# Optimization experiments

Hardware: AMD Instinct MI355X
Metric: run time of the kernel (lower is better)

The kernel has to match this reference:

```python
import jax, jax.numpy as jnp
import numpy as np
from jax import lax

NEG = -jnp.inf


def _lse(x):
    # safe logsumexp over last axis: rows of all -inf give -inf with zero grads
    m = lax.stop_gradient(jnp.max(x, axis=-1, keepdims=True))
    m = jnp.where(jnp.isfinite(m), m, 0.0)
    s = jnp.sum(jnp.exp(x - m), axis=-1)
    return jnp.where(s > 0, jnp.log(jnp.where(s > 0, s, 1.0)), NEG) + m[..., 0]


def _inside(s_arc, s_sib, mask):
    # s_arc[b, dep, head]; s_sib[b, dep, head, sib]; mask[b, s] (col 0 False)
    B, S, _ = s_arc.shape
    A = jnp.transpose(s_arc, (0, 2, 1))        # [b, head, dep]
    SB = jnp.transpose(s_sib, (0, 2, 1, 3))    # [b, head, dep, sib]
    lens = jnp.sum(mask.astype(jnp.int32), axis=1)
    k = jnp.arange(S)[:, None]   # span start index (stripe row)
    j = jnp.arange(S)[None, :]   # offset within stripe (split/sibling)
    d = jnp.arange(S)
    s_i0 = jnp.full((B, S, S), NEG, dtype=s_arc.dtype)  # incomplete spans [b, head, dep]
    s_s0 = s_i0                                          # sibling spans
    s_c0 = s_i0.at[:, d, d].set(0.0)                     # complete spans, width-0 = 0

    def step(carry, w):
        s_i, s_s, s_c = carry
        valid = (k < S - w) & (j < w)
        kw, kj, kj1 = k + w, k + j, k + j + 1
        # left incomplete: I(k+w -> k), siblings at k+1+j
        il = s_i[:, kw, kj1] + s_s[:, kj1, k] + SB[:, kw, k, kj1]
        il = jnp.where(valid, il, NEG)
        il0 = jnp.where(k == 0, 0.0, s_c[:, kw, kw] + s_c[:, k, kw - 1])  # [B,S,1]
        il = jnp.where(j == w - 1, il0, il)
        s_i = jnp.where(k - j == w, _lse(il)[:, None, :] + A, s_i)
        # right incomplete: I(k -> k+w), siblings at k+j (row k=0 forbidden)
        ir = s_i[:, k, kj] + s_s[:, kj, kw] + SB[:, k, kw, kj]
        ir = jnp.where(valid & (k > 0), ir, NEG)
        ir0 = s_c[:, k, k] + s_c[:, kw, k + 1]
        ir = jnp.where(j == 0, ir0, ir)
        s_i = jnp.where(j - k == w, _lse(ir)[:, :, None] + A, s_i)
        # sibling spans S(k, k+w)
        slr = jnp.where(valid, s_c[:, k, kj] + s_c[:, kw, kj1], NEG)
        sl = _lse(slr)
        s_s = jnp.where(k - j == w, sl[:, None, :], s_s)
        s_s = jnp.where(j - k == w, sl[:, :, None], s_s)
        # complete spans (use s_i updated at this width)
        cl = jnp.where(valid, s_c[:, kj, k] + s_i[:, kw, kj], NEG)
        cr = jnp.where(valid, s_i[:, k, kj1] + s_c[:, kj1, kw], NEG)
        s_c = jnp.where(k - j == w, _lse(cl)[:, None, :], s_c)
        s_c = jnp.where(j - k == w, _lse(cr)[:, :, None], s_c)
        # single-root constraint: kill C(0 -> w) for sentences of length != w
        row0 = jnp.where((d[None, :] == w) & (lens[:, None] != w), NEG, s_c[:, 0, :])
        s_c = s_c.at[:, 0, :].set(row0)
        return (s_i, s_s, s_c), None

    (_, _, s_c), _ = lax.scan(jax.checkpoint(step), (s_i0, s_s0, s_c0), jnp.arange(1, S))
    logZ = jnp.take_along_axis(s_c[:, 0, :], lens[:, None], axis=1).sum()
    return logZ


def setup_inputs() -> dict:
    B, S = 16, 128
    key = jax.random.key(0)
    k1, k2, k3, k4 = jax.random.split(key, 4)
    s_arc = jax.random.normal(k1, (B, S, S), jnp.float32)
    s_sib = jax.random.normal(k2, (B, S, S, S), jnp.float32)
    mask = jnp.ones((B, S), bool).at[:, 0].set(False)
    arcs = jax.random.randint(k3, (B, S), 0, S, jnp.int32)
    sibs = jax.random.randint(k4, (B, S, S), 0, S, jnp.int32)
    return {"s_arc": s_arc, "s_sib": s_sib, "mask": mask, "arcs": arcs, "sibs": sibs}


def reference(s_arc, s_sib, mask, arcs, sibs):
    logZ = _inside(s_arc, s_sib, mask)
    arc_sel = jnp.take_along_axis(s_arc, arcs[:, :, None], axis=-1)[..., 0]
    score = jnp.where(mask, arc_sel, 0.0).sum()
    sib_sel = jnp.take_along_axis(s_sib, sibs[..., None], axis=-1)[..., 0]
    score = score + jnp.where(sibs > 0, sib_sel, 0.0).sum()
    loss = (logZ - score) / mask.sum()
    return loss
```

## Files before the change

### kernel.cpp

```cpp
#include <hip/hip_runtime.h>

#define S 128
#define NEGF (-1e30f)
#define MAXB 16
#define NT 1024
#define STAGE_SZ 8064
#define PKB 700000

__device__ float g_ssw[MAXB * S * S];
__device__ float g_spk[(size_t)MAXB * PKB];
__device__ float g_logZ[MAXB];
__device__ float g_partials[512];

__device__ __forceinline__ bool mask_at(const unsigned char* m, int i, bool by) {
  return by ? (m[i] != 0) : (((const int*)m)[i] != 0);
}

__device__ __forceinline__ void gload_lds4(const float* g, float* l) {
  __builtin_amdgcn_global_load_lds(
      (const __attribute__((address_space(1))) unsigned int*)g,
      (__attribute__((address_space(3))) unsigned int*)l, 4, 0, 0);
}

__device__ __forceinline__ void upd(float& m, float& s, float v) {
  float mn = fmaxf(m, v);
  s = s * __expf(m - mn) + __expf(v - mn);
  m = mn;
}
__device__ __forceinline__ void fold(float& m0, float& s0, float m1, float s1) {
  float mn = fmaxf(m0, m1);
  s0 = s0 * __expf(m0 - mn) + s1 * __expf(m1 - mn);
  m0 = mn;
}
template <int CTRL>
__device__ __forceinline__ float dpp_f(float x) {
  int i = __float_as_int(x);
  return __int_as_float(__builtin_amdgcn_update_dpp(i, i, CTRL, 0xF, 0xF, false));
}
__device__ __forceinline__ void xfold(float& m, float& s, int lp) {
  if (lp >= 1) { float mo = dpp_f<0xB1>(m),  so = dpp_f<0xB1>(s);  fold(m, s, mo, so); }
  if (lp >= 2) { float mo = dpp_f<0x4E>(m),  so = dpp_f<0x4E>(s);  fold(m, s, mo, so); }
  if (lp >= 3) { float mo = dpp_f<0x141>(m), so = dpp_f<0x141>(s); fold(m, s, mo, so); }
  if (lp >= 4) { float mo = dpp_f<0x140>(m), so = dpp_f<0x140>(s); fold(m, s, mo, so); }
}
template <typename F>
__device__ __forceinline__ void lse_acc(F val, int i0, int n, float& M, float& Ss) {
  int i = i0;
  const int ie = i0 + n;
  for (; i + 8 <= ie; i += 8) {
    float v0 = val(i),     v1 = val(i + 1), v2 = val(i + 2), v3 = val(i + 3),
          v4 = val(i + 4), v5 = val(i + 5), v6 = val(i + 6), v7 = val(i + 7);
    float mc = fmaxf(fmaxf(fmaxf(v0, v1), fmaxf(v2, v3)),
                     fmaxf(fmaxf(v4, v5), fmaxf(v6, v7)));
    float s8 = ((__expf(v0 - mc) + __expf(v1 - mc)) +
                (__expf(v2 - mc) + __expf(v3 - mc))) +
               ((__expf(v4 - mc) + __expf(v5 - mc)) +
                (__expf(v6 - mc) + __expf(v7 - mc)));
    float mn = fmaxf(M, mc);
    Ss = Ss * __expf(M - mn) + s8 * __expf(mc - mn);
    M = mn;
  }
  for (; i < ie; ++i) upd(M, Ss, val(i));
}
template <typename F>
__device__ __forceinline__ float lse_c8(F val, int i0, int n, int lp) {
  float M = NEGF, Ss = 0.f;
  lse_acc(val, i0, n, M, Ss);
  xfold(M, Ss, lp);
  return __logf(Ss) + M;
}
__device__ __forceinline__ int lp_cap(int cap) {
  return cap >= 16 ? 4 : cap >= 8 ? 3 : cap >= 4 ? 2 : cap >= 2 ? 1 : 0;
}

__global__ __launch_bounds__(256) void pack_kernel(const float* __restrict__ sib) {
  const int wn = 2 + (blockIdx.x % 126);
  const int b = blockIdx.x / 126;
  const int nk2 = S - wn;
  const int rows1 = nk2 - 1;
  if (rows1 <= 0) return;
  const int rowlen = wn - 1;
  const int rlP = rowlen | 1;
  int off = 0;
  for (int v = 2; v < wn; ++v) off += 2 * (S - v - 1) * ((v - 1) | 1);
  const float* SBraw = sib + (size_t)b * S * S * S;
  float* dst = g_spk + (size_t)b * PKB + off;
  const int lane5 = threadIdx.x & 31;
  const int R = 2 * rows1;
  for (int r = (threadIdx.x >> 5); r < R; r += 8) {
    const int typ = (r >= rows1) ? 1 : 0;
    const int kr = (r - typ * rows1) + 1;
    const int kw2 = kr + wn;
    const size_t srcoff = (typ == 0)
        ? ((size_t)(kw2 * S + kr) * S + (kr + 1))
        : ((size_t)(kr * S + kw2) * S + (kr + 1));
    const float* src = SBraw + srcoff;
    float* d = dst + r * rlP;
    for (int i = lane5; i < rowlen; i += 32) d[i] = src[i];
  }
}

__global__ __launch_bounds__(NT) void dp_kernel(
    const float* __restrict__ arc,
    const unsigned char* __restrict__ mask)
{
  __shared__ float si[S][S];
  __shared__ float sc[S][S];
  __shared__ float stage[STAGE_SZ];
  __shared__ int len_sh, cnt0_sh;

  const int b = blockIdx.x;
  const int tid = threadIdx.x;
  const float* arc_b = arc + (size_t)b * S * S;
  const float* spk_b = g_spk + (size_t)b * PKB;
  float* ssw = g_ssw + (size_t)b * S * S;

  if (tid == 0) { len_sh = 0; cnt0_sh = 0; }
  __syncthreads();
  if (tid < S && mask[tid] != 0) atomicAdd(&cnt0_sh, 1);
  for (int i = tid; i < S * S; i += NT) {
    (&si[0][0])[i] = NEGF;
    (&sc[0][0])[i] = NEGF;
  }
  __syncthreads();
  const bool bytes = (cnt0_sh >= 64);
  if (tid < S) {
    sc[tid][tid] = 0.0f;
    if (mask_at(mask, b * S + tid, bytes)) atomicAdd(&len_sh, 1);
  }
  __syncthreads();
  const int len = min(len_sh, S - 1);
  if (tid == 0) g_logZ[b] = 0.0f;

  float mP = NEGF, sP = 0.f, arcvP = 0.f;
  if (tid >= 512) {
    const int fam = (tid >= 768);
    const int floc = tid & 255;
    const int lp = lp_cap(256 / (S - 1));
    const int k = floc >> lp;
    if (k < S - 1)
      arcvP = fam ? arc_b[k * S + (k + 1)] : arc_b[(k + 1) * S + k];
  }

  int spk_off = 0;

  for (int w = 1; w < S; ++w) {
    const int nk = S - w;
    const int wn = w + 1;

    if (wn < S) {
      const int rows1n = S - wn - 1;
      const int T = 2 * rows1n * ((wn - 1) | 1);
      const float* src = spk_b + spk_off;
      const int wv = tid >> 6, l = tid & 63;
      for (int c = wv; c * 64 < T; c += 16) {
        const int e = c * 64 + l;
        if (e < T) gload_lds4(src + e, &stage[c * 64]);
      }
      spk_off += T;
    }

    if (tid < 512) {
      const int lp = lp_cap(512 / nk);
      const int p = 1 << lp;
      const int q = tid & (p - 1);
      const int k = tid >> lp;
      if (k >= 1 && k < nk) {
        const int kw = k + w;
        const float* ra = &sc[k][k];
        const float* rb = &sc[kw][k + 1];
        const int ch = w >> lp;
        const int i0 = q * ch;
        const int n = ((q == p - 1) ? w : i0 + ch) - i0;
        auto val = [&](int i) { return ra[i] + rb[i]; };
        float r = lse_c8(val, i0, n, lp);
        if (q == 0) ssw[w * S + k] = r;
      }
    } else {
      const int fam = (tid >= 768);
      const int floc = tid & 255;
      const int lp = lp_cap(256 / nk);
      const int p = 1 << lp;
      const int q = floc & (p - 1);
      const int k = floc >> lp;
      if (k < nk) {
        const int kw = k + w;
        float bm;
        if (fam == 0) bm = sc[k][k] + sc[kw][k + 1];
        else bm = (k == 0) ? 0.0f : (sc[kw][kw] + sc[k][kw - 1]);
        float m = mP, s = sP;
        if (q == 0) fold(m, s, bm, 1.0f);
        xfold(m, s, lp);
        if (q == 0) {
          const float r = __logf(s) + m + arcvP;
          if (fam == 0) si[k][kw] = r;
          else          si[kw][k] = r;
        }
      }
    }
    __syncthreads();

    if (tid < 512) {
      const int fam = (tid >= 256);
      const int floc = tid & 255;
      const int lp = lp_cap(256 / nk);
      const int p = 1 << lp;
      const int q = floc & (p - 1);
      const int k = floc >> lp;
      if (k < nk) {
        const int kw = k + w;
        const int ch = w >> lp;
        const int i0 = q * ch;
        const int n = ((q == p - 1) ? w : i0 + ch) - i0;
        if (fam == 0) {
          const float* pA = &sc[k][k];
          const float* pB = &si[kw][k];
          auto val = [&](int i) { return pA[i * S] + pB[i]; };
          float r = lse_c8(val, i0, n, lp);
          if (q == 0) sc[kw][k] = r;
        } else {
          const float* pA = &si[k][k + 1];
          const float* pB = &sc[k + 1][kw];
          auto val = [&](int i) { return pA[i] + pB[i * S]; };
          float r = lse_c8(val, i0, n, lp);
          if (q == 0) {
            if (k == 0) {
              if (w == len) g_logZ[b] = r;
              sc[0][w] = (w == len) ? r : NEGF;
            } else {
              sc[k][kw] = r;
            }
          }
        }
      }
    } else {
      mP = NEGF; sP = 0.f; arcvP = 0.f;
      if (wn < S) {
        const int fam = (tid >= 768);
        const int floc = tid & 255;
        const int nk2 = S - wn;
        const int lp = lp_cap(256 / nk2);
        const int p = 1 << lp;
        const int q = floc & (p - 1);
        const int k = floc >> lp;
        if (k < nk2) {
          const int kw2 = k + wn;
          arcvP = (fam == 0) ? arc_b[kw2 * S + k] : arc_b[k * S + kw2];
          if (k >= 1) {
            const int n1n = wn - 1;
            const int rlPn = n1n | 1;
            const float *pa, *pt, *pw;
            int wstr;
            if (fam == 0) {
              pa = &si[k][k + 1];
              pt = &stage[(k - 1) * rlPn];
              pw = ssw + n1n * S + (k + 1);
              wstr = 1 - S;
            } else {
              pa = &si[kw2][k + 1];
              pt = &stage[((nk2 - 1) + (k - 1)) * rlPn];
              pw = ssw + S + k;
              wstr = S;
            }
            const int ch = n1n >> lp;
            const int i0 = q * ch;
            const int n = ((q == p - 1) ? n1n : i0 + ch) - i0;
            auto val = [&](int i) { return pa[i] + pt[i] + pw[i * wstr]; };
            lse_acc(val, i0, n, mP, sP);
          }
        }
      }
    }
    __syncthreads();
  }
}

__global__ __launch_bounds__(256) void score_kernel(
    const float* __restrict__ arc, const float* __restrict__ sib,
    const unsigned char* __restrict__ mask, const int* __restrict__ arcs,
    const int* __restrict__ sibs, int B)
{
  __shared__ bool bytes_sh;
  if (threadIdx.x == 0) {
    int c = 0;
    for (int i = 0; i < S; ++i) c += (mask[i] != 0);
    bytes_sh = (c >= 64);
  }
  __syncthreads();
  const bool bytes = bytes_sh;

  const int total = B * S * S;
  int tid = blockIdx.x * blockDim.x + threadIdx.x;
  float sum = 0.f, cnt = 0.f;
  for (int e = tid; e < total; e += gridDim.x * blockDim.x) {
    int sv = sibs[e];
    if (sv > 0) sum += sib[(size_t)e * S + sv];
    if ((e & (S - 1)) == 0) {
      int bi = e >> 7;
      if (mask_at(mask, bi, bytes)) { sum += arc[(size_t)bi * S + arcs[bi]]; cnt += 1.f; }
    }
  }
  __shared__ float rs[256], rc[256];
  rs[threadIdx.x] = sum; rc[threadIdx.x] = cnt;
  __syncthreads();
  for (int off = 128; off; off >>= 1) {
    if (threadIdx.x < off) {
      rs[threadIdx.x] += rs[threadIdx.x + off];
      rc[threadIdx.x] += rc[threadIdx.x + off];
    }
    __syncthreads();
  }
  if (threadIdx.x == 0) {
    g_partials[blockIdx.x * 2]     = rs[0];
    g_partials[blockIdx.x * 2 + 1] = rc[0];
  }
}

__global__ __launch_bounds__(256) void final_kernel(int B, float* __restrict__ out)
{
  __shared__ float rs[256], rc[256];
  int t = threadIdx.x;
  float v = -g_partials[t * 2];
  float c = g_partials[t * 2 + 1];
  if (t < B) v += g_logZ[t];
  rs[t] = v; rc[t] = c;
  __syncthreads();
  for (int off = 128; off; off >>= 1) {
    if (t < off) { rs[t] += rs[t + off]; rc[t] += rc[t + off]; }
    __syncthreads();
  }
  if (t == 0) out[0] = rs[0] / rc[0];
}

extern "C" void kernel_launch(void* const* d_in, const int* in_sizes, int n_in,
                              void* d_out, int out_size, void* d_ws, size_t ws_size,
                              hipStream_t stream) {
  const float* s_arc = (const float*)d_in[0];
  const float* s_sib = (const float*)d_in[1];
  const unsigned char* mask = (const unsigned char*)d_in[2];
  const int* arcs = (const int*)d_in[3];
  const int* sibs = (const int*)d_in[4];
  int B = in_sizes[0] / (S * S);
  if (B > MAXB) B = MAXB;

  pack_kernel<<<dim3(B * 126), dim3(256), 0, stream>>>(s_sib);
  score_kernel<<<dim3(256), dim3(256), 0, stream>>>(s_arc, s_sib, mask, arcs, sibs, B);
  dp_kernel<<<dim3(B), dim3(NT), 0, stream>>>(s_arc, mask);
  final_kernel<<<dim3(1), dim3(256), 0, stream>>>(B, (float*)d_out);
}
```

Before: 547.3 us.

## Transpose packed sibling scores and read them directly from global memory

The pack kernel now writes sibling scores transposed, with an LDS tile transpose, so that consecutive k values are contiguous for each split index i. The DP kernel drops the per-width global-to-LDS staging buffer and its async loads and reads the packed data straight from global memory, so lanes over k coalesce. The accumulation helpers are also respecialised with compile-time strides instead of lambdas. This removes LDS staging traffic and shared-memory footprint but puts global-memory latency directly on the inner lse loop and grows the packed buffer.

```diff
diff --git a/kernel.cpp b/kernel.cpp
--- a/kernel.cpp
+++ b/kernel.cpp
@@ -4,22 +4,15 @@
 #define NEGF (-1e30f)
 #define MAXB 16
 #define NT 1024
-#define STAGE_SZ 8064
-#define PKB 700000
+#define PKB2 2080000
 
 __device__ float g_ssw[MAXB * S * S];
-__device__ float g_spk[(size_t)MAXB * PKB];
+__device__ float g_spk2[(size_t)MAXB * PKB2];
 __device__ float g_logZ[MAXB];
 __device__ float g_partials[512];
 
 __device__ __forceinline__ bool mask_at(const unsigned char* m, int i, bool by) {
   return by ? (m[i] != 0) : (((const int*)m)[i] != 0);
-}
-
-__device__ __forceinline__ void gload_lds4(const float* g, float* l) {
-  __builtin_amdgcn_global_load_lds(
-      (const __attribute__((address_space(1))) unsigned int*)g,
-      (__attribute__((address_space(3))) unsigned int*)l, 4, 0, 0);
 }
 
 __device__ __forceinline__ void upd(float& m, float& s, float v) {
@@ -43,13 +36,23 @@
   if (lp >= 3) { float mo = dpp_f<0x141>(m), so = dpp_f<0x141>(s); fold(m, s, mo, so); }
   if (lp >= 4) { float mo = dpp_f<0x140>(m), so = dpp_f<0x140>(s); fold(m, s, mo, so); }
 }
-template <typename F>
-__device__ __forceinline__ void lse_acc(F val, int i0, int n, float& M, float& Ss) {
-  int i = i0;
-  const int ie = i0 + n;
-  for (; i + 8 <= ie; i += 8) {
-    float v0 = val(i),     v1 = val(i + 1), v2 = val(i + 2), v3 = val(i + 3),
-          v4 = val(i + 4), v5 = val(i + 5), v6 = val(i + 6), v7 = val(i + 7);
+__device__ __forceinline__ int lp_cap(int cap) {
+  return cap >= 16 ? 4 : cap >= 8 ? 3 : cap >= 4 ? 2 : cap >= 2 ? 1 : 0;
+}
+
+template <int SA, int SB>
+__device__ __forceinline__ void acc2(const float* a, const float* b,
+                                     int n, float& M, float& Ss) {
+  int i = 0;
+  for (; i + 8 <= n; i += 8) {
+    float v0 = a[0 * SA] + b[0 * SB];
+    float v1 = a[1 * SA] + b[1 * SB];
+    float v2 = a[2 * SA] + b[2 * SB];
+    float v3 = a[3 * SA] + b[3 * SB];
+    float v4 = a[4 * SA] + b[4 * SB];
+    float v5 = a[5 * SA] + b[5 * SB];
+    float v6 = a[6 * SA] + b[6 * SB];
+    float v7 = a[7 * SA] + b[7 * SB];
     float mc = fmaxf(fmaxf(fmaxf(v0, v1), fmaxf(v2, v3)),
                      fmaxf(fmaxf(v4, v5), fmaxf(v6, v7)));
     float s8 = ((__expf(v0 - mc) + __expf(v1 - mc)) +
@@ -59,44 +62,69 @@
     float mn = fmaxf(M, mc);
     Ss = Ss * __expf(M - mn) + s8 * __expf(mc - mn);
     M = mn;
-  }
-  for (; i < ie; ++i) upd(M, Ss, val(i));
-}
-template <typename F>
-__device__ __forceinline__ float lse_c8(F val, int i0, int n, int lp) {
-  float M = NEGF, Ss = 0.f;
-  lse_acc(val, i0, n, M, Ss);
-  xfold(M, Ss, lp);
-  return __logf(Ss) + M;
-}
-__device__ __forceinline__ int lp_cap(int cap) {
-  return cap >= 16 ? 4 : cap >= 8 ? 3 : cap >= 4 ? 2 : cap >= 2 ? 1 : 0;
+    a += 8 * SA; b += 8 * SB;
+  }
+  for (; i < n; ++i) { upd(M, Ss, a[0] + b[0]); a += SA; b += SB; }
+}
+template <int SA, int SB, int SC_>
+__device__ __forceinline__ void acc3(const float* a, const float* b,
+                                     const float* c, int n, float& M, float& Ss) {
+  int i = 0;
+  for (; i + 8 <= n; i += 8) {
+    float v0 = a[0 * SA] + b[0 * SB] + c[0 * SC_];
+    float v1 = a[1 * SA] + b[1 * SB] + c[1 * SC_];
+    float v2 = a[2 * SA] + b[2 * SB] + c[2 * SC_];
+    float v3 = a[3 * SA] + b[3 * SB] + c[3 * SC_];
+    float v4 = a[4 * SA] + b[4 * SB] + c[4 * SC_];
+    float v5 = a[5 * SA] + b[5 * SB] + c[5 * SC_];
+    float v6 = a[6 * SA] + b[6 * SB] + c[6 * SC_];
+    float v7 = a[7 * SA] + b[7 * SB] + c[7 * SC_];
+    float mc = fmaxf(fmaxf(fmaxf(v0, v1), fmaxf(v2, v3)),
+                     fmaxf(fmaxf(v4, v5), fmaxf(v6, v7)));
+    float s8 = ((__expf(v0 - mc) + __expf(v1 - mc)) +
+                (__expf(v2 - mc) + __expf(v3 - mc))) +
+               ((__expf(v4 - mc) + __expf(v5 - mc)) +
+                (__expf(v6 - mc) + __expf(v7 - mc)));
+    float mn = fmaxf(M, mc);
+    Ss = Ss * __expf(M - mn) + s8 * __expf(mc - mn);
+    M = mn;
+    a += 8 * SA; b += 8 * SB; c += 8 * SC_;
+  }
+  for (; i < n; ++i) { upd(M, Ss, a[0] + b[0] + c[0]); a += SA; b += SB; c += SC_; }
 }
 
 __global__ __launch_bounds__(256) void pack_kernel(const float* __restrict__ sib) {
   const int wn = 2 + (blockIdx.x % 126);
   const int b = blockIdx.x / 126;
   const int nk2 = S - wn;
-  const int rows1 = nk2 - 1;
-  if (rows1 <= 0) return;
-  const int rowlen = wn - 1;
-  const int rlP = rowlen | 1;
-  int off = 0;
-  for (int v = 2; v < wn; ++v) off += 2 * (S - v - 1) * ((v - 1) | 1);
+  const int R = nk2 - 1;
+  if (R <= 0) return;
+  const int I = wn - 1;
   const float* SBraw = sib + (size_t)b * S * S * S;
-  float* dst = g_spk + (size_t)b * PKB + off;
-  const int lane5 = threadIdx.x & 31;
-  const int R = 2 * rows1;
-  for (int r = (threadIdx.x >> 5); r < R; r += 8) {
-    const int typ = (r >= rows1) ? 1 : 0;
-    const int kr = (r - typ * rows1) + 1;
-    const int kw2 = kr + wn;
-    const size_t srcoff = (typ == 0)
-        ? ((size_t)(kw2 * S + kr) * S + (kr + 1))
-        : ((size_t)(kr * S + kw2) * S + (kr + 1));
-    const float* src = SBraw + srcoff;
-    float* d = dst + r * rlP;
-    for (int i = lane5; i < rowlen; i += 32) d[i] = src[i];
+  float* dst0 = g_spk2 + (size_t)b * PKB2 + (size_t)128 * (wn - 1) * (wn - 2);
+  __shared__ float tile[32][33];
+  const int tx = threadIdx.x & 31, ty = threadIdx.x >> 5;
+  for (int typ = 0; typ < 2; ++typ) {
+    float* dst = dst0 + (size_t)typ * I * 128;
+    for (int bi = 0; bi < I; bi += 32) {
+      for (int bk = 0; bk < R; bk += 32) {
+        for (int yy = ty; yy < 32; yy += 8) {
+          int kk = bk + yy, i = bi + tx;
+          if (kk < R && i < I) {
+            int k = kk + 1, kw2 = k + wn;
+            size_t srow = (typ == 0) ? ((size_t)(kw2 * S + k) * S)
+                                     : ((size_t)(k * S + kw2) * S);
+            tile[yy][tx] = SBraw[srow + (k + 1 + i)];
+          }
+        }
+        __syncthreads();
+        for (int yy = ty; yy < 32; yy += 8) {
+          int i = bi + yy, kk = bk + tx;
+          if (i < I && kk < R) dst[(size_t)i * 128 + kk] = tile[tx][yy];
+        }
+        __syncthreads();
+      }
+    }
   }
 }
 
@@ -106,13 +134,12 @@
 {
   __shared__ float si[S][S];
   __shared__ float sc[S][S];
-  __shared__ float stage[STAGE_SZ];
   __shared__ int len_sh, cnt0_sh;
 
   const int b = blockIdx.x;
   const int tid = threadIdx.x;
   const float* arc_b = arc + (size_t)b * S * S;
-  const float* spk_b = g_spk + (size_t)b * PKB;
+  const float* spk_b = g_spk2 + (size_t)b * PKB2;
   float* ssw = g_ssw + (size_t)b * S * S;
 
   if (tid == 0) { len_sh = 0; cnt0_sh = 0; }
@@ -142,23 +169,9 @@
       arcvP = fam ? arc_b[k * S + (k + 1)] : arc_b[(k + 1) * S + k];
   }
 
-  int spk_off = 0;
-
   for (int w = 1; w < S; ++w) {
     const int nk = S - w;
     const int wn = w + 1;
-
-    if (wn < S) {
-      const int rows1n = S - wn - 1;
-      const int T = 2 * rows1n * ((wn - 1) | 1);
-      const float* src = spk_b + spk_off;
-      const int wv = tid >> 6, l = tid & 63;
-      for (int c = wv; c * 64 < T; c += 16) {
-        const int e = c * 64 + l;
-        if (e < T) gload_lds4(src + e, &stage[c * 64]);
-      }
-      spk_off += T;
-    }
 
     if (tid < 512) {
       const int lp = lp_cap(512 / nk);
@@ -167,14 +180,13 @@
       const int k = tid >> lp;
       if (k >= 1 && k < nk) {
         const int kw = k + w;
-        const float* ra = &sc[k][k];
-        const float* rb = &sc[kw][k + 1];
         const int ch = w >> lp;
         const int i0 = q * ch;
         const int n = ((q == p - 1) ? w : i0 + ch) - i0;
-        auto val = [&](int i) { return ra[i] + rb[i]; };
-        float r = lse_c8(val, i0, n, lp);
-        if (q == 0) ssw[w * S + k] = r;
+        float M = NEGF, Ss = 0.f;
+        acc2<1, 1>(&sc[k][k] + i0, &sc[kw][k + 1] + i0, n, M, Ss);
+        xfold(M, Ss, lp);
+        if (q == 0) ssw[w * S + k] = __logf(Ss) + M;
       }
     } else {
       const int fam = (tid >= 768);
@@ -212,18 +224,16 @@
         const int ch = w >> lp;
         const int i0 = q * ch;
         const int n = ((q == p - 1) ? w : i0 + ch) - i0;
+        float M = NEGF, Ss = 0.f;
         if (fam == 0) {
-          const float* pA = &sc[k][k];
-          const float* pB = &si[kw][k];
-          auto val = [&](int i) { return pA[i * S] + pB[i]; };
-          float r = lse_c8(val, i0, n, lp);
-          if (q == 0) sc[kw][k] = r;
+          acc2<S, 1>(&sc[k + i0][k], &si[kw][k] + i0, n, M, Ss);
+          xfold(M, Ss, lp);
+          if (q == 0) sc[kw][k] = __logf(Ss) + M;
         } else {
-          const float* pA = &si[k][k + 1];
-          const float* pB = &sc[k + 1][kw];
-          auto val = [&](int i) { return pA[i] + pB[i * S]; };
-          float r = lse_c8(val, i0, n, lp);
+          acc2<1, S>(&si[k][k + 1] + i0, &sc[k + 1 + i0][kw], n, M, Ss);
+          xfold(M, Ss, lp);
           if (q == 0) {
+            const float r = __logf(Ss) + M;
             if (k == 0) {
               if (w == len) g_logZ[b] = r;
               sc[0][w] = (w == len) ? r : NEGF;
@@ -248,25 +258,20 @@
           arcvP = (fam == 0) ? arc_b[kw2 * S + k] : arc_b[k * S + kw2];
           if (k >= 1) {
             const int n1n = wn - 1;
-            const int rlPn = n1n | 1;
-            const float *pa, *pt, *pw;
-            int wstr;
-            if (fam == 0) {
-              pa = &si[k][k + 1];
-              pt = &stage[(k - 1) * rlPn];
-              pw = ssw + n1n * S + (k + 1);
-              wstr = 1 - S;
-            } else {
-              pa = &si[kw2][k + 1];
-              pt = &stage[((nk2 - 1) + (k - 1)) * rlPn];
-              pw = ssw + S + k;
-              wstr = S;
-            }
+            const float* pk = spk_b + (size_t)128 * (wn - 1) * (wn - 2)
+                              + (size_t)fam * n1n * 128 + (k - 1);
             const int ch = n1n >> lp;
             const int i0 = q * ch;
             const int n = ((q == p - 1) ? n1n : i0 + ch) - i0;
-            auto val = [&](int i) { return pa[i] + pt[i] + pw[i * wstr]; };
-            lse_acc(val, i0, n, mP, sP);
+            if (fam == 0) {
+              acc3<1, 1 - S, 128>(&si[k][k + 1] + i0,
+                                  ssw + (wn - 1) * S + (k + 1) + i0 * (1 - S),
+                                  pk + (size_t)i0 * 128, n, mP, sP);
+            } else {
+              acc3<1, S, 128>(&si[kw2][k + 1] + i0,
+                              ssw + S + k + i0 * S,
+                              pk + (size_t)i0 * 128, n, mP, sP);
+            }
           }
         }
       }
```

Result: slower. 619.3 us (+13.2%).
